# Optimization experiments

Measured on AMD Instinct MI355X. Metric: run time of the kernel, lower is better.

## Reference

```python
import math
import jax, jax.numpy as jnp
import numpy as np

RCR = 5.2
RCA = 3.5
ETA_R = 16.0
ETA_A = 8.0
ZETA = 32.0
NUM_SPECIES = 4
SHF_R = jnp.linspace(0.9, RCR, 17)[:-1]                      # [16]
SHF_A = jnp.linspace(0.9, RCA, 5)[:-1]                       # [4]
SHF_Z = (jnp.linspace(0.0, math.pi, 9) + math.pi / 16)[:-1]  # [8]


def _triu_index(num_species):
    i1, i2 = np.triu_indices(num_species)
    pair = np.arange(len(i1))
    ret = np.zeros((num_species, num_species), dtype=np.int32)
    ret[i1, i2] = pair
    ret[i2, i1] = pair
    return jnp.asarray(ret)

TRIU = _triu_index(NUM_SPECIES)  # [S,S] -> pair index in [0, S(S+1)/2)


def setup_inputs() -> dict:
    key = jax.random.key(0)
    k1, k2 = jax.random.split(key)
    species = jax.random.randint(k1, (64, 32), 0, NUM_SPECIES, dtype=jnp.int32)
    # spread atoms over a few Angstrom so neighbor lists are non-trivial
    coordinates = jax.random.normal(k2, (64, 32, 3), dtype=jnp.float32) * 2.0
    return {"species": species, "coordinates": coordinates}


def _cutoff_cosine(d, rc):
    # CutoffCosine: 0.5*cos(pi*d/rc)+0.5 inside cutoff, 0 outside
    return jnp.where(d <= rc, 0.5 * jnp.cos(math.pi * d / rc) + 0.5, 0.0)


def _aev(species, coordinates):
    N, A, _ = coordinates.shape
    S = NUM_SPECIES
    # vec[n,i,j] = coords[n,j] - coords[n,i]
    diff = coordinates[:, None, :, :] - coordinates[:, :, None, :]  # [N,A,A,3]
    d2 = jnp.sum(diff * diff, axis=-1)                              # [N,A,A]
    dist = jnp.sqrt(jnp.where(d2 > 0, d2, 1.0))
    eye = jnp.eye(A, dtype=bool)

    # ---- radial AEV: 0.25 * exp(-EtaR*(d-ShfR)^2) * fc(d), binned by species[j]
    rmask = (~eye) & (dist <= RCR)                                  # [N,A,A]
    fc_r = _cutoff_cosine(dist, RCR)
    g = 0.25 * jnp.exp(-ETA_R * (dist[..., None] - SHF_R) ** 2) * fc_r[..., None]
    g = g * rmask[..., None]                                        # [N,A,A,16]
    sp_onehot = jax.nn.one_hot(species, S, dtype=g.dtype)           # [N,A,S]
    radial = jnp.einsum('nijr,njs->nisr', g, sp_onehot).reshape(N, A, S * 16)

    # ---- angular AEV over triplets (i; j<k), both neighbors within Rca
    amask = (~eye) & (dist <= RCA)                                  # [N,A,A]
    fc_a = _cutoff_cosine(dist, RCA) * amask
    dot = jnp.einsum('nijc,nikc->nijk', diff, diff)                 # [N,A,A,A]
    denom = dist[:, :, :, None] * dist[:, :, None, :]
    cos_ang = jnp.clip(0.95 * dot / jnp.where(denom > 0, denom, 1.0), -0.95, 0.95)
    theta = jnp.arccos(cos_ang)                                     # [N,A,A,A]
    dmean = 0.5 * (dist[:, :, :, None] + dist[:, :, None, :])
    f1 = ((1.0 + jnp.cos(theta[..., None] - SHF_Z)) * 0.5) ** ZETA  # [N,A,A,A,8]
    f2 = jnp.exp(-ETA_A * (dmean[..., None] - SHF_A) ** 2)          # [N,A,A,A,4]
    jk = jnp.arange(A)
    tmask = amask[:, :, :, None] & amask[:, :, None, :] & (jk[:, None] < jk[None, :])
    fc_pair = fc_a[:, :, :, None] * fc_a[:, :, None, :] * tmask
    # sublength ordering: ShfA outer, ShfZ inner (EtaA, Zeta are scalars)
    term = 2.0 * f2[..., :, None] * f1[..., None, :]                # [N,A,A,A,4,8]
    term = (term * fc_pair[..., None, None]).reshape(N, A, A, A, 32)
    pair_idx = TRIU[species[:, :, None], species[:, None, :]]       # [N,A,A]
    pair_oh = jax.nn.one_hot(pair_idx, S * (S + 1) // 2, dtype=term.dtype)
    angular = jnp.einsum('nijku,njkp->nipu', term, pair_oh)
    angular = angular.reshape(N, A, (S * (S + 1) // 2) * 32)

    return jnp.concatenate([radial, angular], axis=-1)              # [N,A,384]


def reference(species, coordinates):
    aev = _aev(species, coordinates)
    return species, aev
```

## Files before the change

### kernel.cpp

```cpp
#include <hip/hip_runtime.h>
#include <math.h>

#define NATOMS 32
#define NMOL   64
#define MAXP   466
#define RCRf 5.2f
#define RCAf 3.5f

__global__ __launch_bounds__(384) void aev_kernel(const int* __restrict__ species,
                                                  const float* __restrict__ coords,
                                                  float* __restrict__ out) {
    const int bid = blockIdx.x;
    const int n = bid >> 5;
    const int i = bid & 31;
    const int tid = threadIdx.x;

    __shared__ float4 s_atom[NATOMS];
    __shared__ float  s_fca[NATOMS], s_fcr[NATOMS];
    __shared__ int    s_sp[NATOMS];
    __shared__ int    s_nbr[NATOMS];
    __shared__ int    s_nn;
    __shared__ __align__(16) float s_rec[MAXP*12];
    __shared__ int    s_cnt[10], s_base[10], s_ofs[10];

    if (tid < 10) s_cnt[tid] = 0;

    if (tid < 64) {
        float fca_v = 0.f;
        if (tid < NATOMS) {
            const float* cb = coords + (size_t)n*NATOMS*3;
            float dx = cb[tid*3+0] - cb[i*3+0];
            float dy = cb[tid*3+1] - cb[i*3+1];
            float dz = cb[tid*3+2] - cb[i*3+2];
            float d2 = dx*dx + dy*dy + dz*dz;
            float d  = sqrtf(d2 > 0.f ? d2 : 1.f);
            bool self = (tid == i);
            s_fcr[tid] = (!self && d <= RCRf) ? (0.5f*__cosf(((float)M_PI/RCRf)*d) + 0.5f) : 0.f;
            fca_v      = (!self && d <= RCAf) ? (0.5f*__cosf(((float)M_PI/RCAf)*d) + 0.5f) : 0.f;
            s_fca[tid]  = fca_v;
            s_atom[tid] = make_float4(dx, dy, dz, d);
            s_sp[tid]   = species[n*NATOMS + tid];
        }
        unsigned long long m = __ballot(fca_v > 0.f);
        if (fca_v > 0.f) s_nbr[__popcll(m & ((1ull << tid) - 1ull))] = tid;
        if (tid == 0) s_nn = (int)__popcll(m);
    }
    __syncthreads();

    const int nn  = s_nn;
    const int cnt = (nn*(nn-1)) >> 1;
    const int M   = 2*nn - 1;

    int pj[2] = {-1, -1}, pk[2], ppx[2];
    #pragma unroll
    for (int rep = 0; rep < 2; ++rep) {
        int p = tid + rep*384;
        if (p < cnt) {
            float t = sqrtf((float)(M*M - 8*p));
            int jj = (int)(((float)M - t) * 0.5f);
            while (jj*(2*nn-jj-1)/2 > p) --jj;
            while ((jj+1)*(2*nn-jj-2)/2 <= p) ++jj;
            int kk = p - jj*(2*nn-jj-1)/2 + jj + 1;
            int j = s_nbr[jj], k = s_nbr[kk];
            int sj = s_sp[j], sk = s_sp[k];
            int lo = min(sj, sk), hi = max(sj, sk);
            int px = ((lo*(9-lo)) >> 1) + (hi - lo);
            pj[rep] = j; pk[rep] = k; ppx[rep] = px;
            atomicAdd(&s_cnt[px], 1);
        }
    }
    __syncthreads();

    if (tid == 0) {
        int run = 0;
        #pragma unroll
        for (int b = 0; b < 10; ++b) { s_base[b] = run; s_ofs[b] = run; run += s_cnt[b]; }
    }
    __syncthreads();

    const float CZ[8] = { 0.98078528f,  0.83146961f,  0.55557023f,  0.19509032f,
                         -0.19509032f, -0.55557023f, -0.83146961f, -0.98078528f};
    const float SZ[8] = { 0.19509032f,  0.55557023f,  0.83146961f,  0.98078528f,
                          0.98078528f,  0.83146961f,  0.55557023f,  0.19509032f};
    const float SHA[4] = {0.9f, 1.55f, 2.2f, 2.85f};

    #pragma unroll
    for (int rep = 0; rep < 2; ++rep) {
        if (pj[rep] >= 0) {
            int j = pj[rep], k = pk[rep];
            float4 aj = s_atom[j], ak = s_atom[k];
            float fc2 = 2.f * s_fca[j] * s_fca[k];
            float dot = aj.x*ak.x + aj.y*ak.y + aj.z*ak.z;
            float c = 0.95f * dot * __builtin_amdgcn_rcpf(aj.w * ak.w);
            c = fminf(0.95f, fmaxf(-0.95f, c));
            float s = sqrtf(1.f - c*c);
            float dmean = 0.5f * (aj.w + ak.w);
            float f1[8], f2f[4];
            #pragma unroll
            for (int z = 0; z < 8; ++z) {
                float x = 0.5f + 0.5f*(c*CZ[z] + s*SZ[z]);
                float q = x*x; q *= q; q *= q; q *= q; q *= q;
                f1[z] = q;
            }
            #pragma unroll
            for (int a = 0; a < 4; ++a) {
                float dm = dmean - SHA[a];
                f2f[a] = __expf(-8.f*dm*dm) * fc2;
            }
            int slot = atomicAdd(&s_ofs[ppx[rep]], 1);
            float* r = &s_rec[slot*12];
            *(float4*)(r+0) = make_float4(f1[0], f1[1], f1[2], f1[3]);
            *(float4*)(r+4) = make_float4(f1[4], f1[5], f1[6], f1[7]);
            *(float4*)(r+8) = make_float4(f2f[0], f2f[1], f2f[2], f2f[3]);
        }
    }
    __syncthreads();

    float* oa = out + NMOL*NATOMS + (size_t)bid * 384;

    if (tid < 320) {
        const int b = tid >> 5;
        const int a = (tid >> 3) & 3;
        const int z = tid & 7;
        const int p0 = s_base[b];
        const int pe = p0 + s_cnt[b];
        float acc = 0.f;
        #pragma unroll 4
        for (int p = p0; p < pe; ++p)
            acc += s_rec[p*12 + z] * s_rec[p*12 + 8 + a];
        oa[64 + tid] = acc;
    } else {
        const int f  = tid - 320;
        const int rs = f >> 4;
        const float shr = 0.9f + 0.26875f * (float)(f & 15);
        float racc = 0.f;
        #pragma unroll 8
        for (int j = 0; j < NATOMS; ++j) {
            float d = s_atom[j].w, fr = s_fcr[j];
            float dmr = d - shr;
            racc += (s_sp[j] == rs) ? 0.25f * __expf(-16.f*dmr*dmr) * fr : 0.f;
        }
        oa[f] = racc;
        if (f == 0) out[bid] = (float)s_sp[i];
    }
}

extern "C" void kernel_launch(void* const* d_in, const int* in_sizes, int n_in,
                              void* d_out, int out_size, void* d_ws, size_t ws_size,
                              hipStream_t stream) {
    const int*   species = (const int*)d_in[0];
    const float* coords  = (const float*)d_in[1];
    float*       out     = (float*)d_out;
    aev_kernel<<<NMOL * NATOMS, 384, 0, stream>>>(species, coords, out);
}
```

Measured before the change: 16.10 us.

## Replace atomic pair bucketing with masked full scan over all triplets

Drops the counting-sort stage (shared atomics, prefix sum by one thread, two barriers) that grouped angular triplets by species pair. Each triplet record is now written at its own index along with its pair id, and each accumulator thread scans every triplet, keeping only those whose pair id matches its bucket. This removes serialized atomics and synchronization, at the cost of each thread scanning up to ten times more records from shared memory. Radial inputs are also packed into a float2 and the species output write moves to thread 0.

```diff
diff --git a/kernel.cpp b/kernel.cpp
--- a/kernel.cpp
+++ b/kernel.cpp
@@ -16,14 +16,13 @@
     const int tid = threadIdx.x;
 
     __shared__ float4 s_atom[NATOMS];
-    __shared__ float  s_fca[NATOMS], s_fcr[NATOMS];
+    __shared__ float2 s_dfr[NATOMS];
+    __shared__ float  s_fca[NATOMS];
     __shared__ int    s_sp[NATOMS];
     __shared__ int    s_nbr[NATOMS];
     __shared__ int    s_nn;
     __shared__ __align__(16) float s_rec[MAXP*12];
-    __shared__ int    s_cnt[10], s_base[10], s_ofs[10];
-
-    if (tid < 10) s_cnt[tid] = 0;
+    __shared__ int    s_px[MAXP];
 
     if (tid < 64) {
         float fca_v = 0.f;
@@ -35,10 +34,11 @@
             float d2 = dx*dx + dy*dy + dz*dz;
             float d  = sqrtf(d2 > 0.f ? d2 : 1.f);
             bool self = (tid == i);
-            s_fcr[tid] = (!self && d <= RCRf) ? (0.5f*__cosf(((float)M_PI/RCRf)*d) + 0.5f) : 0.f;
-            fca_v      = (!self && d <= RCAf) ? (0.5f*__cosf(((float)M_PI/RCAf)*d) + 0.5f) : 0.f;
+            float fr = (!self && d <= RCRf) ? (0.5f*__cosf(((float)M_PI/RCRf)*d) + 0.5f) : 0.f;
+            fca_v    = (!self && d <= RCAf) ? (0.5f*__cosf(((float)M_PI/RCAf)*d) + 0.5f) : 0.f;
+            s_atom[tid] = make_float4(dx, dy, dz, d);
+            s_dfr[tid]  = make_float2(d, fr);
             s_fca[tid]  = fca_v;
-            s_atom[tid] = make_float4(dx, dy, dz, d);
             s_sp[tid]   = species[n*NATOMS + tid];
         }
         unsigned long long m = __ballot(fca_v > 0.f);
@@ -51,33 +51,6 @@
     const int cnt = (nn*(nn-1)) >> 1;
     const int M   = 2*nn - 1;
 
-    int pj[2] = {-1, -1}, pk[2], ppx[2];
-    #pragma unroll
-    for (int rep = 0; rep < 2; ++rep) {
-        int p = tid + rep*384;
-        if (p < cnt) {
-            float t = sqrtf((float)(M*M - 8*p));
-            int jj = (int)(((float)M - t) * 0.5f);
-            while (jj*(2*nn-jj-1)/2 > p) --jj;
-            while ((jj+1)*(2*nn-jj-2)/2 <= p) ++jj;
-            int kk = p - jj*(2*nn-jj-1)/2 + jj + 1;
-            int j = s_nbr[jj], k = s_nbr[kk];
-            int sj = s_sp[j], sk = s_sp[k];
-            int lo = min(sj, sk), hi = max(sj, sk);
-            int px = ((lo*(9-lo)) >> 1) + (hi - lo);
-            pj[rep] = j; pk[rep] = k; ppx[rep] = px;
-            atomicAdd(&s_cnt[px], 1);
-        }
-    }
-    __syncthreads();
-
-    if (tid == 0) {
-        int run = 0;
-        #pragma unroll
-        for (int b = 0; b < 10; ++b) { s_base[b] = run; s_ofs[b] = run; run += s_cnt[b]; }
-    }
-    __syncthreads();
-
     const float CZ[8] = { 0.98078528f,  0.83146961f,  0.55557023f,  0.19509032f,
                          -0.19509032f, -0.55557023f, -0.83146961f, -0.98078528f};
     const float SZ[8] = { 0.19509032f,  0.55557023f,  0.83146961f,  0.98078528f,
@@ -86,8 +59,15 @@
 
     #pragma unroll
     for (int rep = 0; rep < 2; ++rep) {
-        if (pj[rep] >= 0) {
-            int j = pj[rep], k = pk[rep];
+        int p = tid + rep*384;
+        if (p < cnt) {
+            float t = sqrtf((float)(M*M - 8*p));
+            int jj = (int)(((float)M - t) * 0.5f);
+            jj = max(0, min(jj, nn-2));
+            while (jj*(2*nn-jj-1)/2 > p) --jj;
+            while ((jj+1)*(2*nn-jj-2)/2 <= p) ++jj;
+            int kk = p - jj*(2*nn-jj-1)/2 + jj + 1;
+            int j = s_nbr[jj], k = s_nbr[kk];
             float4 aj = s_atom[j], ak = s_atom[k];
             float fc2 = 2.f * s_fca[j] * s_fca[k];
             float dot = aj.x*ak.x + aj.y*ak.y + aj.z*ak.z;
@@ -95,23 +75,32 @@
             c = fminf(0.95f, fmaxf(-0.95f, c));
             float s = sqrtf(1.f - c*c);
             float dmean = 0.5f * (aj.w + ak.w);
-            float f1[8], f2f[4];
-            #pragma unroll
-            for (int z = 0; z < 8; ++z) {
-                float x = 0.5f + 0.5f*(c*CZ[z] + s*SZ[z]);
-                float q = x*x; q *= q; q *= q; q *= q; q *= q;
-                f1[z] = q;
-            }
-            #pragma unroll
-            for (int a = 0; a < 4; ++a) {
-                float dm = dmean - SHA[a];
-                f2f[a] = __expf(-8.f*dm*dm) * fc2;
-            }
-            int slot = atomicAdd(&s_ofs[ppx[rep]], 1);
-            float* r = &s_rec[slot*12];
-            *(float4*)(r+0) = make_float4(f1[0], f1[1], f1[2], f1[3]);
-            *(float4*)(r+4) = make_float4(f1[4], f1[5], f1[6], f1[7]);
-            *(float4*)(r+8) = make_float4(f2f[0], f2f[1], f2f[2], f2f[3]);
+            int sj = s_sp[j], sk = s_sp[k];
+            int lo = min(sj, sk), hi = max(sj, sk);
+            float* r = &s_rec[p*12];
+            float4 v0, v1, v2;
+            v0.x = 0.5f + 0.5f*(c*CZ[0] + s*SZ[0]);
+            v0.y = 0.5f + 0.5f*(c*CZ[1] + s*SZ[1]);
+            v0.z = 0.5f + 0.5f*(c*CZ[2] + s*SZ[2]);
+            v0.w = 0.5f + 0.5f*(c*CZ[3] + s*SZ[3]);
+            v1.x = 0.5f + 0.5f*(c*CZ[4] + s*SZ[4]);
+            v1.y = 0.5f + 0.5f*(c*CZ[5] + s*SZ[5]);
+            v1.z = 0.5f + 0.5f*(c*CZ[6] + s*SZ[6]);
+            v1.w = 0.5f + 0.5f*(c*CZ[7] + s*SZ[7]);
+            #define POW32(q) { q = q*q; q = q*q; q = q*q; q = q*q; q = q*q; }
+            POW32(v0.x) POW32(v0.y) POW32(v0.z) POW32(v0.w)
+            POW32(v1.x) POW32(v1.y) POW32(v1.z) POW32(v1.w)
+            #undef POW32
+            float dm0 = dmean - SHA[0], dm1 = dmean - SHA[1];
+            float dm2 = dmean - SHA[2], dm3 = dmean - SHA[3];
+            v2.x = __expf(-8.f*dm0*dm0) * fc2;
+            v2.y = __expf(-8.f*dm1*dm1) * fc2;
+            v2.z = __expf(-8.f*dm2*dm2) * fc2;
+            v2.w = __expf(-8.f*dm3*dm3) * fc2;
+            *(float4*)(r+0) = v0;
+            *(float4*)(r+4) = v1;
+            *(float4*)(r+8) = v2;
+            s_px[p] = ((lo*(9-lo)) >> 1) + (hi - lo);
         }
     }
     __syncthreads();
@@ -122,13 +111,16 @@
         const int b = tid >> 5;
         const int a = (tid >> 3) & 3;
         const int z = tid & 7;
-        const int p0 = s_base[b];
-        const int pe = p0 + s_cnt[b];
         float acc = 0.f;
         #pragma unroll 4
-        for (int p = p0; p < pe; ++p)
-            acc += s_rec[p*12 + z] * s_rec[p*12 + 8 + a];
+        for (int p = 0; p < cnt; ++p) {
+            int   px = s_px[p];
+            float f1 = s_rec[p*12 + z];
+            float f2 = s_rec[p*12 + 8 + a];
+            acc += (px == b) ? f1*f2 : 0.f;
+        }
         oa[64 + tid] = acc;
+        if (tid == 0) out[bid] = (float)s_sp[i];
     } else {
         const int f  = tid - 320;
         const int rs = f >> 4;
@@ -136,12 +128,11 @@
         float racc = 0.f;
         #pragma unroll 8
         for (int j = 0; j < NATOMS; ++j) {
-            float d = s_atom[j].w, fr = s_fcr[j];
-            float dmr = d - shr;
-            racc += (s_sp[j] == rs) ? 0.25f * __expf(-16.f*dmr*dmr) * fr : 0.f;
+            float2 dfr = s_dfr[j];
+            float dmr = dfr.x - shr;
+            racc += (s_sp[j] == rs) ? 0.25f * __expf(-16.f*dmr*dmr) * dfr.y : 0.f;
         }
         oa[f] = racc;
-        if (f == 0) out[bid] = (float)s_sp[i];
     }
 }
 
```

After: 21.10 us. 1.31x slower.
